# Kernel optimization log

Measured on AMD Instinct MI355X. Metric: run time of the kernel, lower is better.

## Reference

```python
import jax, jax.numpy as jnp
import numpy as np

B, CIN, COUT, H, W = 16, 128, 128, 64, 64
K1, K2, DIL = 3, 3, 1
PAD0 = DIL * (K1 - 1) // 2
PAD1 = DIL * (K2 - 1) // 2
L = H * W


def setup_inputs() -> dict:
    key = jax.random.key(0)
    k1, k2, k3, k4, k5 = jax.random.split(key, 5)
    x = jax.random.normal(k1, (B, CIN, H, W), dtype=jnp.float32)
    # binary per-pixel mask over kernel taps, broadcast over batch*channels
    mask = (jax.random.uniform(k2, (1, K1 * K2, L)) < 0.5).astype(jnp.float32)
    fan_in = CIN * K1 * K2
    bound = 1.0 / np.sqrt(fan_in)
    weight = jax.random.uniform(k3, (COUT, CIN, K1, K2), jnp.float32, -bound, bound)
    mask_weight = jax.random.uniform(k4, (COUT, K1, K2), jnp.float32, -bound, bound)
    bias = jax.random.uniform(k5, (COUT,), jnp.float32, -bound, bound)
    return {"x": x, "mask": mask, "weight": weight, "mask_weight": mask_weight, "bias": bias}


def reference(x, mask, weight, mask_weight, bias):
    # im2col: [B, CIN*K1*K2, H, W]; channel ordering (cin, k1, k2) matches torch unfold
    patches = jax.lax.conv_general_dilated_patches(
        x, (K1, K2), (1, 1), [(PAD0, PAD0), (PAD1, PAD1)], rhs_dilation=(DIL, DIL))
    p = patches.reshape(B, CIN, K1 * K2, L)
    p = p * mask[:, None, :, :]          # mask [1, K, L] broadcasts over B and CIN
    p = p.reshape(B, CIN * K1 * K2, L)
    out = jnp.einsum('ok,bkl->bol', weight.reshape(COUT, -1), p)
    out = out + bias[None, :, None]
    out = out + jnp.einsum('ok,mkl->mol', mask_weight.reshape(COUT, -1), mask)
    return out.reshape(B, COUT, H, W)
```

## Files before the change

kernel.cpp:

```cpp
#include <hip/hip_runtime.h>
#include <stdint.h>

#define B_    16
#define CIN_  128
#define COUT_ 128
#define H_    64
#define W_    64
#define L_    4096
#define KK_   1152
#define PW_   66
#define PPIX_ (PW_ * PW_)

typedef unsigned short u16;
typedef __bf16 bf16x8 __attribute__((ext_vector_type(8)));
typedef float  floatx4 __attribute__((ext_vector_type(4)));
typedef uint32_t u32x4 __attribute__((ext_vector_type(4)));

typedef const __attribute__((address_space(1))) uint32_t* gptr_t;
typedef __attribute__((address_space(3))) uint32_t*       lptr_t;

__device__ __forceinline__ void async_copy16(const void* g, void* l) {
    __builtin_amdgcn_global_load_lds((gptr_t)g, (lptr_t)l, 16, 0, 0);
}

__device__ __forceinline__ u16 f2bf(float f) {
    uint32_t u = __builtin_bit_cast(uint32_t, f);
    uint32_t r = u + 0x7FFFu + ((u >> 16) & 1u);
    return (u16)(r >> 16);
}

__global__ void lmc_prep_kernel(const float* __restrict__ x,
                                const float* __restrict__ mask, const float* __restrict__ mw,
                                const float* __restrict__ bias, const float* __restrict__ w,
                                u16* __restrict__ xTp, float* __restrict__ mb,
                                u16* __restrict__ wb2) {
    const int bid = blockIdx.x, tid = threadIdx.x;
    if (bid < 1024) {
        __shared__ u16 tile[64][CIN_ + 8];
        const int b = bid >> 6;
        const int y = bid & 63;

        {
            const int c  = tid >> 1;
            const int x0 = (tid & 1) * 32;
            const float* src = x + ((size_t)b * CIN_ + c) * L_ + y * 64 + x0;
            #pragma unroll
            for (int j = 0; j < 32; j += 4) {
                float4 v = *reinterpret_cast<const float4*>(src + j);
                tile[x0 + j + 0][c] = f2bf(v.x);
                tile[x0 + j + 1][c] = f2bf(v.y);
                tile[x0 + j + 2][c] = f2bf(v.z);
                tile[x0 + j + 3][c] = f2bf(v.w);
            }
        }
        __syncthreads();

        u16* dstrow = xTp + ((size_t)(b * PW_ + (y + 1)) * PW_) * CIN_;
        {
            const int xx   = tid >> 2;
            const int cseg = (tid & 3) * 32;
            u16* dst = dstrow + (size_t)(xx + 1) * CIN_ + cseg;
            #pragma unroll
            for (int i = 0; i < 32; i += 8) {
                *reinterpret_cast<uint4*>(dst + i) =
                    *reinterpret_cast<const uint4*>(&tile[xx][cseg + i]);
            }
        }
        const uint4 z = {0u, 0u, 0u, 0u};
        if (tid < 32) {
            const int pix = (tid >> 4) ? 65 : 0;
            *reinterpret_cast<uint4*>(dstrow + (size_t)pix * CIN_ + (tid & 15) * 8) = z;
        }
        if (y == 0 || y == 63) {
            u16* brow = xTp + ((size_t)(b * PW_ + (y == 0 ? 0 : 65)) * PW_) * CIN_;
            for (int i = tid; i < (PW_ * CIN_) / 8; i += 256)
                reinterpret_cast<uint4*>(brow)[i] = z;
        }
    } else if (bid < 1152) {
        const int o = bid - 1024;
        float m[9];
        #pragma unroll
        for (int k = 0; k < 9; ++k) m[k] = mw[o * 9 + k];
        const float bs = bias[o];
        for (int l = tid; l < L_; l += 256) {
            float s = bs;
            #pragma unroll
            for (int k = 0; k < 9; ++k) s += m[k] * mask[k * L_ + l];
            mb[o * L_ + l] = s;
        }
    } else {
        const int base = (bid - 1152) * 2304;
        #pragma unroll
        for (int i = 0; i < 9; ++i) {
            const int e = base + i * 256 + tid;
            const int k = e >> 14;
            const int rem = e & 16383;
            const int o = rem >> 7, c = rem & 127;
            wb2[e] = f2bf(w[(size_t)o * KK_ + c * 9 + k]);
        }
    }
}

__global__ __launch_bounds__(512, 2)
void lmc_gemm_kernel(const u16* __restrict__ xTp, const u16* __restrict__ wb2,
                     const float* __restrict__ mask, const float* __restrict__ mb,
                     float* __restrict__ out) {
    __shared__ u16 W_lds[396 * 128];
    __shared__ u16 A_lds[3][128 * 64];

    const int flat    = blockIdx.x;
    const int logical = (flat & 7) * 32 + (flat >> 3);
    const int b       = logical >> 4;
    const int lt      = logical & 15;
    const int Y       = lt * 4;
    const int l0      = lt * 256;

    const int tid  = threadIdx.x;
    const int lane = tid & 63;
    const int wv   = tid >> 6;
    const int wm   = (wv >> 2) * 64;
    const int wn   = (wv & 3) * 64;
    const int lrow = lane & 15;
    const int quad = lane >> 4;

    const char* wb2_c = (const char*)wb2;
    char* A_c = (char*)A_lds;

    {
        const char* xw = (const char*)xTp + ((size_t)(b * PW_ + Y) * PW_) * 256;
        for (int t = wv; t < 99; t += 8) {
            const int p    = t * 4 + quad;
            const int srcc = lrow ^ (p & 7);
            async_copy16(xw + (size_t)p * 256 + srcc * 16,
                         (char*)W_lds + t * 1024);
        }
    }

    const int ao  = (lane >> 3);
    const int ach = (lane & 7) ^ (ao & 7);
    const int aoff0 = (8 * wv + ao) * 256 + ach * 16;
    async_copy16(wb2_c + aoff0,              A_c + wv * 1024);
    async_copy16(wb2_c + aoff0 + 16384,      A_c + wv * 1024 + 8192);
    async_copy16(wb2_c + 128 + aoff0,        A_c + 16384 + wv * 1024);
    async_copy16(wb2_c + 128 + aoff0 + 16384, A_c + 16384 + wv * 1024 + 8192);

    int pix0[4];
    uint64_t bits = 0;
    #pragma unroll
    for (int j = 0; j < 4; ++j) {
        const int ll = wn + j * 16 + lrow;
        pix0[j] = ((ll >> 6) + 1) * 66 + (ll & 63) + 1;
        const int lg = l0 + ll;
        #pragma unroll
        for (int k = 0; k < 9; ++k)
            if (mask[k * L_ + lg] != 0.0f) bits |= (1ull << (k * 4 + j));
    }

    floatx4 acc[4][4];
    #pragma unroll
    for (int i = 0; i < 4; ++i)
        #pragma unroll
        for (int j = 0; j < 4; ++j)
            acc[i][j] = (floatx4){0.f, 0.f, 0.f, 0.f};

    asm volatile("s_waitcnt vmcnt(2)" ::: "memory");
    __builtin_amdgcn_s_barrier();
    asm volatile("" ::: "memory");

    int bufr = 0;
    int bufw = 2;
    for (int g = 0; g < 18; ++g) {
        const int k = g >> 1;

        if (g < 16) {
            const int gn   = g + 2;
            const int koff = (gn >> 1) * 32768 + (gn & 1) * 128;
            char* dstb = A_c + bufw * 16384;
            async_copy16(wb2_c + koff + aoff0,         dstb + wv * 1024);
            async_copy16(wb2_c + koff + aoff0 + 16384, dstb + wv * 1024 + 8192);
        }

        const int sh = (k / 3 - 1) * 66 + (k % 3) - 1;
        uint32_t kp[4];
        #pragma unroll
        for (int j = 0; j < 4; ++j)
            kp[j] = 0u - (uint32_t)((bits >> (k * 4 + j)) & 1ull);

        const u16* Ac = (const u16*)(A_c + bufr * 16384);

        #pragma unroll
        for (int ksl = 0; ksl < 2; ++ksl) {
            const int ksg = (g & 1) * 2 + ksl;
            bf16x8 af[4], bf[4];
            #pragma unroll
            for (int i = 0; i < 4; ++i) {
                const int orow = wm + i * 16 + lrow;
                const int slot = (ksl * 4 + quad) ^ (orow & 7);
                af[i] = *reinterpret_cast<const bf16x8*>(&Ac[orow * 64 + slot * 8]);
            }
            #pragma unroll
            for (int j = 0; j < 4; ++j) {
                const int pix  = pix0[j] + sh;
                const int slot = (ksg * 4 + quad) ^ (pix & 7);
                bf16x8 v = *reinterpret_cast<const bf16x8*>(&W_lds[pix * 128 + slot * 8]);
                u32x4 t = __builtin_bit_cast(u32x4, v);
                t &= kp[j];
                bf[j] = __builtin_bit_cast(bf16x8, t);
            }
            __builtin_amdgcn_s_setprio(1);
            #pragma unroll
            for (int i = 0; i < 4; ++i)
                #pragma unroll
                for (int j = 0; j < 4; ++j)
                    acc[i][j] = __builtin_amdgcn_mfma_f32_16x16x32_bf16(
                        af[i], bf[j], acc[i][j], 0, 0, 0);
            __builtin_amdgcn_s_setprio(0);
        }

        if (g < 16) {
            asm volatile("s_waitcnt vmcnt(2)" ::: "memory");
            __builtin_amdgcn_s_barrier();
            asm volatile("" ::: "memory");
        } else if (g == 16) {
            asm volatile("s_waitcnt vmcnt(0)" ::: "memory");
            __builtin_amdgcn_s_barrier();
            asm volatile("" ::: "memory");
        }
        bufr = (bufr == 2) ? 0 : bufr + 1;
        bufw = (bufw == 2) ? 0 : bufw + 1;
    }

    #pragma unroll
    for (int i = 0; i < 4; ++i) {
        #pragma unroll
        for (int j = 0; j < 4; ++j) {
            const int l = l0 + wn + j * 16 + lrow;
            #pragma unroll
            for (int r = 0; r < 4; ++r) {
                const int o = wm + i * 16 + quad * 4 + r;
                out[((size_t)b * COUT_ + o) * L_ + l] = acc[i][j][r] + mb[o * L_ + l];
            }
        }
    }
}

extern "C" void kernel_launch(void* const* d_in, const int* in_sizes, int n_in,
                              void* d_out, int out_size, void* d_ws, size_t ws_size,
                              hipStream_t stream) {
    const float* x      = (const float*)d_in[0];
    const float* mask   = (const float*)d_in[1];
    const float* weight = (const float*)d_in[2];
    const float* mw     = (const float*)d_in[3];
    const float* bias   = (const float*)d_in[4];
    float* out = (float*)d_out;

    char* ws = (char*)d_ws;
    u16*   xTp = (u16*)ws;
    u16*   wb2 = (u16*)(ws + 17842176);
    float* mb  = (float*)(ws + 17842176 + 294912);

    lmc_prep_kernel<<<1216, 256, 0, stream>>>(x, mask, mw, bias, weight, xTp, mb, wb2);
    lmc_gemm_kernel<<<256, 512, 0, stream>>>(xTp, wb2, mask, mb, out);
}
```

Baseline: 124.7 us.

## Fuse prep and GEMM kernels into one cooperative kernel with grid sync

Merges the separate prep kernel (bf16 transpose/padding of x, mask-bias precompute, weight reorder) into the GEMM kernel. Each of the 256 blocks does its share of the prep work and then waits at a grid-wide barrier before the GEMM phase. This is meant to remove one kernel launch and the gap between the two kernels. In exchange, prep now runs on only 256 blocks instead of 1216, and the grid barrier adds a synchronization cost.

```diff
diff --git a/kernel.cpp b/kernel.cpp
--- a/kernel.cpp
+++ b/kernel.cpp
@@ -1,5 +1,8 @@
 #include <hip/hip_runtime.h>
+#include <hip/hip_cooperative_groups.h>
 #include <stdint.h>
+
+namespace cg = cooperative_groups;
 
 #define B_    16
 #define CIN_  128
@@ -29,82 +32,12 @@
     return (u16)(r >> 16);
 }
 
-__global__ void lmc_prep_kernel(const float* __restrict__ x,
-                                const float* __restrict__ mask, const float* __restrict__ mw,
-                                const float* __restrict__ bias, const float* __restrict__ w,
-                                u16* __restrict__ xTp, float* __restrict__ mb,
-                                u16* __restrict__ wb2) {
-    const int bid = blockIdx.x, tid = threadIdx.x;
-    if (bid < 1024) {
-        __shared__ u16 tile[64][CIN_ + 8];
-        const int b = bid >> 6;
-        const int y = bid & 63;
-
-        {
-            const int c  = tid >> 1;
-            const int x0 = (tid & 1) * 32;
-            const float* src = x + ((size_t)b * CIN_ + c) * L_ + y * 64 + x0;
-            #pragma unroll
-            for (int j = 0; j < 32; j += 4) {
-                float4 v = *reinterpret_cast<const float4*>(src + j);
-                tile[x0 + j + 0][c] = f2bf(v.x);
-                tile[x0 + j + 1][c] = f2bf(v.y);
-                tile[x0 + j + 2][c] = f2bf(v.z);
-                tile[x0 + j + 3][c] = f2bf(v.w);
-            }
-        }
-        __syncthreads();
-
-        u16* dstrow = xTp + ((size_t)(b * PW_ + (y + 1)) * PW_) * CIN_;
-        {
-            const int xx   = tid >> 2;
-            const int cseg = (tid & 3) * 32;
-            u16* dst = dstrow + (size_t)(xx + 1) * CIN_ + cseg;
-            #pragma unroll
-            for (int i = 0; i < 32; i += 8) {
-                *reinterpret_cast<uint4*>(dst + i) =
-                    *reinterpret_cast<const uint4*>(&tile[xx][cseg + i]);
-            }
-        }
-        const uint4 z = {0u, 0u, 0u, 0u};
-        if (tid < 32) {
-            const int pix = (tid >> 4) ? 65 : 0;
-            *reinterpret_cast<uint4*>(dstrow + (size_t)pix * CIN_ + (tid & 15) * 8) = z;
-        }
-        if (y == 0 || y == 63) {
-            u16* brow = xTp + ((size_t)(b * PW_ + (y == 0 ? 0 : 65)) * PW_) * CIN_;
-            for (int i = tid; i < (PW_ * CIN_) / 8; i += 256)
-                reinterpret_cast<uint4*>(brow)[i] = z;
-        }
-    } else if (bid < 1152) {
-        const int o = bid - 1024;
-        float m[9];
-        #pragma unroll
-        for (int k = 0; k < 9; ++k) m[k] = mw[o * 9 + k];
-        const float bs = bias[o];
-        for (int l = tid; l < L_; l += 256) {
-            float s = bs;
-            #pragma unroll
-            for (int k = 0; k < 9; ++k) s += m[k] * mask[k * L_ + l];
-            mb[o * L_ + l] = s;
-        }
-    } else {
-        const int base = (bid - 1152) * 2304;
-        #pragma unroll
-        for (int i = 0; i < 9; ++i) {
-            const int e = base + i * 256 + tid;
-            const int k = e >> 14;
-            const int rem = e & 16383;
-            const int o = rem >> 7, c = rem & 127;
-            wb2[e] = f2bf(w[(size_t)o * KK_ + c * 9 + k]);
-        }
-    }
-}
-
 __global__ __launch_bounds__(512, 2)
-void lmc_gemm_kernel(const u16* __restrict__ xTp, const u16* __restrict__ wb2,
-                     const float* __restrict__ mask, const float* __restrict__ mb,
-                     float* __restrict__ out) {
+void lmc_fused_kernel(const float* __restrict__ x,
+                      const float* __restrict__ mask, const float* __restrict__ mw,
+                      const float* __restrict__ bias, const float* __restrict__ w,
+                      u16* __restrict__ xTp, float* __restrict__ mb,
+                      u16* __restrict__ wb2, float* __restrict__ out) {
     __shared__ u16 W_lds[396 * 128];
     __shared__ u16 A_lds[3][128 * 64];
 
@@ -123,6 +56,82 @@
     const int lrow = lane & 15;
     const int quad = lane >> 4;
 
+    {
+        u16* tile = (u16*)W_lds;
+        const uint4 z = {0u, 0u, 0u, 0u};
+        for (int r = 0; r < 4; ++r) {
+            const int y = Y + r;
+            {
+                const int c  = tid >> 2;
+                const int x0 = (tid & 3) * 16;
+                const float* src = x + ((size_t)b * CIN_ + c) * L_ + y * 64 + x0;
+                #pragma unroll
+                for (int j = 0; j < 16; j += 4) {
+                    float4 v = *reinterpret_cast<const float4*>(src + j);
+                    tile[(x0 + j + 0) * 136 + c] = f2bf(v.x);
+                    tile[(x0 + j + 1) * 136 + c] = f2bf(v.y);
+                    tile[(x0 + j + 2) * 136 + c] = f2bf(v.z);
+                    tile[(x0 + j + 3) * 136 + c] = f2bf(v.w);
+                }
+            }
+            __syncthreads();
+            u16* dstrow = xTp + ((size_t)(b * PW_ + (y + 1)) * PW_) * CIN_;
+            {
+                const int xx = tid >> 3;
+                const int cs = (tid & 7) * 16;
+                u16* dst = dstrow + (size_t)(xx + 1) * CIN_ + cs;
+                *reinterpret_cast<uint4*>(dst)     = *reinterpret_cast<const uint4*>(&tile[xx * 136 + cs]);
+                *reinterpret_cast<uint4*>(dst + 8) = *reinterpret_cast<const uint4*>(&tile[xx * 136 + cs + 8]);
+            }
+            if (tid < 32) {
+                const int pix = (tid >> 4) ? 65 : 0;
+                *reinterpret_cast<uint4*>(dstrow + (size_t)pix * CIN_ + (tid & 15) * 8) = z;
+            }
+            __syncthreads();
+        }
+        if (lt == 0 || lt == 15) {
+            u16* brow = xTp + ((size_t)(b * PW_ + (lt == 0 ? 0 : 65)) * PW_) * CIN_;
+            for (int i = tid; i < (PW_ * CIN_) / 8; i += 512)
+                reinterpret_cast<uint4*>(brow)[i] = z;
+        }
+    }
+
+    {
+        const int o  = flat >> 1;
+        const int l  = (flat & 1) * 2048 + tid * 4;
+        float m[9];
+        #pragma unroll
+        for (int k = 0; k < 9; ++k) m[k] = mw[o * 9 + k];
+        const float bs = bias[o];
+        float4 s = {bs, bs, bs, bs};
+        #pragma unroll
+        for (int k = 0; k < 9; ++k) {
+            float4 mk = *reinterpret_cast<const float4*>(&mask[k * L_ + l]);
+            s.x += m[k] * mk.x;  s.y += m[k] * mk.y;
+            s.z += m[k] * mk.z;  s.w += m[k] * mk.w;
+        }
+        *reinterpret_cast<float4*>(&mb[o * L_ + l]) = s;
+    }
+
+    {
+        const int e0 = flat * 576 + tid;
+        {
+            const int e = e0;
+            const int k = e >> 14, rem = e & 16383;
+            const int o = rem >> 7, c = rem & 127;
+            wb2[e] = f2bf(w[(size_t)o * KK_ + c * 9 + k]);
+        }
+        if (tid < 64) {
+            const int e = e0 + 512;
+            const int k = e >> 14, rem = e & 16383;
+            const int o = rem >> 7, c = rem & 127;
+            wb2[e] = f2bf(w[(size_t)o * KK_ + c * 9 + k]);
+        }
+    }
+
+    __threadfence();
+    cg::this_grid().sync();
+
     const char* wb2_c = (const char*)wb2;
     char* A_c = (char*)A_lds;
 
@@ -139,9 +148,9 @@
     const int ao  = (lane >> 3);
     const int ach = (lane & 7) ^ (ao & 7);
     const int aoff0 = (8 * wv + ao) * 256 + ach * 16;
-    async_copy16(wb2_c + aoff0,              A_c + wv * 1024);
-    async_copy16(wb2_c + aoff0 + 16384,      A_c + wv * 1024 + 8192);
-    async_copy16(wb2_c + 128 + aoff0,        A_c + 16384 + wv * 1024);
+    async_copy16(wb2_c + aoff0,               A_c + wv * 1024);
+    async_copy16(wb2_c + aoff0 + 16384,       A_c + wv * 1024 + 8192);
+    async_copy16(wb2_c + 128 + aoff0,         A_c + 16384 + wv * 1024);
     async_copy16(wb2_c + 128 + aoff0 + 16384, A_c + 16384 + wv * 1024 + 8192);
 
     int pix0[4];
@@ -259,6 +268,8 @@
     u16*   wb2 = (u16*)(ws + 17842176);
     float* mb  = (float*)(ws + 17842176 + 294912);
 
-    lmc_prep_kernel<<<1216, 256, 0, stream>>>(x, mask, mw, bias, weight, xTp, mb, wb2);
-    lmc_gemm_kernel<<<256, 512, 0, stream>>>(xTp, wb2, mask, mb, out);
-}
+    void* args[] = {(void*)&x, (void*)&mask, (void*)&mw, (void*)&bias, (void*)&weight,
+                    (void*)&xTp, (void*)&mb, (void*)&wb2, (void*)&out};
+    hipLaunchCooperativeKernel((const void*)lmc_fused_kernel,
+                               dim3(256), dim3(512), args, 0, stream);
+}
```

Measured after the change: 225.9 us. +81.2%, slower.

## Fuse x bf16 transpose/padding into GEMM kernel, loading fp32 x directly into LDS

Applied to the files above, without the earlier changes.

Removes the prep-kernel stage that converted x to a padded, channel-last bf16 buffer in workspace. The GEMM kernel now reads fp32 x directly, converts it to bf16 in registers and writes it swizzled into LDS, zeroing the halo itself. This drops a full write and re-read of the intermediate tensor and shrinks the prep launch. In exchange the input load is synchronous instead of async-to-LDS, so it no longer overlaps with the first weight loads. Halo rows are also read redundantly across tiles.

```diff
diff --git a/kernel.cpp b/kernel.cpp
--- a/kernel.cpp
+++ b/kernel.cpp
@@ -8,8 +8,6 @@
 #define W_    64
 #define L_    4096
 #define KK_   1152
-#define PW_   66
-#define PPIX_ (PW_ * PW_)
 
 typedef unsigned short u16;
 typedef __bf16 bf16x8 __attribute__((ext_vector_type(8)));
@@ -29,55 +27,12 @@
     return (u16)(r >> 16);
 }
 
-__global__ void lmc_prep_kernel(const float* __restrict__ x,
-                                const float* __restrict__ mask, const float* __restrict__ mw,
+__global__ void lmc_prep_kernel(const float* __restrict__ mask, const float* __restrict__ mw,
                                 const float* __restrict__ bias, const float* __restrict__ w,
-                                u16* __restrict__ xTp, float* __restrict__ mb,
-                                u16* __restrict__ wb2) {
+                                float* __restrict__ mb, u16* __restrict__ wb2) {
     const int bid = blockIdx.x, tid = threadIdx.x;
-    if (bid < 1024) {
-        __shared__ u16 tile[64][CIN_ + 8];
-        const int b = bid >> 6;
-        const int y = bid & 63;
-
-        {
-            const int c  = tid >> 1;
-            const int x0 = (tid & 1) * 32;
-            const float* src = x + ((size_t)b * CIN_ + c) * L_ + y * 64 + x0;
-            #pragma unroll
-            for (int j = 0; j < 32; j += 4) {
-                float4 v = *reinterpret_cast<const float4*>(src + j);
-                tile[x0 + j + 0][c] = f2bf(v.x);
-                tile[x0 + j + 1][c] = f2bf(v.y);
-                tile[x0 + j + 2][c] = f2bf(v.z);
-                tile[x0 + j + 3][c] = f2bf(v.w);
-            }
-        }
-        __syncthreads();
-
-        u16* dstrow = xTp + ((size_t)(b * PW_ + (y + 1)) * PW_) * CIN_;
-        {
-            const int xx   = tid >> 2;
-            const int cseg = (tid & 3) * 32;
-            u16* dst = dstrow + (size_t)(xx + 1) * CIN_ + cseg;
-            #pragma unroll
-            for (int i = 0; i < 32; i += 8) {
-                *reinterpret_cast<uint4*>(dst + i) =
-                    *reinterpret_cast<const uint4*>(&tile[xx][cseg + i]);
-            }
-        }
-        const uint4 z = {0u, 0u, 0u, 0u};
-        if (tid < 32) {
-            const int pix = (tid >> 4) ? 65 : 0;
-            *reinterpret_cast<uint4*>(dstrow + (size_t)pix * CIN_ + (tid & 15) * 8) = z;
-        }
-        if (y == 0 || y == 63) {
-            u16* brow = xTp + ((size_t)(b * PW_ + (y == 0 ? 0 : 65)) * PW_) * CIN_;
-            for (int i = tid; i < (PW_ * CIN_) / 8; i += 256)
-                reinterpret_cast<uint4*>(brow)[i] = z;
-        }
-    } else if (bid < 1152) {
-        const int o = bid - 1024;
+    if (bid < 128) {
+        const int o = bid;
         float m[9];
         #pragma unroll
         for (int k = 0; k < 9; ++k) m[k] = mw[o * 9 + k];
@@ -89,7 +44,7 @@
             mb[o * L_ + l] = s;
         }
     } else {
-        const int base = (bid - 1152) * 2304;
+        const int base = (bid - 128) * 2304;
         #pragma unroll
         for (int i = 0; i < 9; ++i) {
             const int e = base + i * 256 + tid;
@@ -102,7 +57,7 @@
 }
 
 __global__ __launch_bounds__(512, 2)
-void lmc_gemm_kernel(const u16* __restrict__ xTp, const u16* __restrict__ wb2,
+void lmc_gemm_kernel(const float* __restrict__ x, const u16* __restrict__ wb2,
                      const float* __restrict__ mask, const float* __restrict__ mb,
                      float* __restrict__ out) {
     __shared__ u16 W_lds[396 * 128];
@@ -123,26 +78,55 @@
     const int lrow = lane & 15;
     const int quad = lane >> 4;
 
-    const char* wb2_c = (const char*)wb2;
-    char* A_c = (char*)A_lds;
-
+    if (tid < 192) {
+        const int h  = tid >> 4;
+        const int px = (h >> 1) * 66 + ((h & 1) ? 65 : 0);
+        const uint4 z = {0u, 0u, 0u, 0u};
+        *reinterpret_cast<uint4*>((char*)W_lds + px * 256 + (tid & 15) * 16) = z;
+    }
     {
-        const char* xw = (const char*)xTp + ((size_t)(b * PW_ + Y) * PW_) * 256;
-        for (int t = wv; t < 99; t += 8) {
-            const int p    = t * 4 + quad;
-            const int srcc = lrow ^ (p & 7);
-            async_copy16(xw + (size_t)p * 256 + srcc * 16,
-                         (char*)W_lds + t * 1024);
-        }
-    }
-
-    const int ao  = (lane >> 3);
-    const int ach = (lane & 7) ^ (ao & 7);
-    const int aoff0 = (8 * wv + ao) * 256 + ach * 16;
-    async_copy16(wb2_c + aoff0,              A_c + wv * 1024);
-    async_copy16(wb2_c + aoff0 + 16384,      A_c + wv * 1024 + 8192);
-    async_copy16(wb2_c + 128 + aoff0,        A_c + 16384 + wv * 1024);
-    async_copy16(wb2_c + 128 + aoff0 + 16384, A_c + 16384 + wv * 1024 + 8192);
+        const int cg  = lane >> 4;
+        const int x0  = (lane & 15) * 4;
+        const int cb  = wv;
+        const int cbase = cb * 16 + cg * 4;
+        const int d     = cb * 2 + (cg >> 1);
+        const int half8 = (cg & 1) * 8;
+        const float* xc = x + ((size_t)(b * CIN_ + cbase) * L_) + x0;
+
+        #pragma unroll
+        for (int wy = 0; wy < 6; ++wy) {
+            const int y   = Y - 1 + wy;
+            const int px0 = wy * 66 + x0 + 1;
+            if (y >= 0 && y <= 63) {
+                const float* xr = xc + y * 64;
+                float4 v0 = *reinterpret_cast<const float4*>(xr);
+                float4 v1 = *reinterpret_cast<const float4*>(xr + L_);
+                float4 v2 = *reinterpret_cast<const float4*>(xr + 2 * L_);
+                float4 v3 = *reinterpret_cast<const float4*>(xr + 3 * L_);
+                const float* p0 = (const float*)&v0;
+                const float* p1 = (const float*)&v1;
+                const float* p2 = (const float*)&v2;
+                const float* p3 = (const float*)&v3;
+                #pragma unroll
+                for (int j = 0; j < 4; ++j) {
+                    const int px   = px0 + j;
+                    const int slot = d ^ (px & 7);
+                    uint2 pk;
+                    pk.x = (uint32_t)f2bf(p0[j]) | ((uint32_t)f2bf(p1[j]) << 16);
+                    pk.y = (uint32_t)f2bf(p2[j]) | ((uint32_t)f2bf(p3[j]) << 16);
+                    *reinterpret_cast<uint2*>((char*)W_lds + px * 256 + slot * 16 + half8) = pk;
+                }
+            } else {
+                const uint2 z2 = {0u, 0u};
+                #pragma unroll
+                for (int j = 0; j < 4; ++j) {
+                    const int px   = px0 + j;
+                    const int slot = d ^ (px & 7);
+                    *reinterpret_cast<uint2*>((char*)W_lds + px * 256 + slot * 16 + half8) = z2;
+                }
+            }
+        }
+    }
 
     int pix0[4];
     uint64_t bits = 0;
@@ -156,6 +140,16 @@
             if (mask[k * L_ + lg] != 0.0f) bits |= (1ull << (k * 4 + j));
     }
 
+    const char* wb2_c = (const char*)wb2;
+    char* A_c = (char*)A_lds;
+    const int ao  = (lane >> 3);
+    const int ach = (lane & 7) ^ (ao & 7);
+    const int aoff0 = (8 * wv + ao) * 256 + ach * 16;
+    async_copy16(wb2_c + aoff0,               A_c + wv * 1024);
+    async_copy16(wb2_c + aoff0 + 16384,       A_c + wv * 1024 + 8192);
+    async_copy16(wb2_c + 128 + aoff0,         A_c + 16384 + wv * 1024);
+    async_copy16(wb2_c + 128 + aoff0 + 16384, A_c + 16384 + wv * 1024 + 8192);
+
     floatx4 acc[4][4];
     #pragma unroll
     for (int i = 0; i < 4; ++i)
@@ -163,7 +157,7 @@
         for (int j = 0; j < 4; ++j)
             acc[i][j] = (floatx4){0.f, 0.f, 0.f, 0.f};
 
-    asm volatile("s_waitcnt vmcnt(2)" ::: "memory");
+    asm volatile("s_waitcnt vmcnt(2) lgkmcnt(0)" ::: "memory");
     __builtin_amdgcn_s_barrier();
     asm volatile("" ::: "memory");
 
@@ -255,10 +249,9 @@
     float* out = (float*)d_out;
 
     char* ws = (char*)d_ws;
-    u16*   xTp = (u16*)ws;
-    u16*   wb2 = (u16*)(ws + 17842176);
-    float* mb  = (float*)(ws + 17842176 + 294912);
-
-    lmc_prep_kernel<<<1216, 256, 0, stream>>>(x, mask, mw, bias, weight, xTp, mb, wb2);
-    lmc_gemm_kernel<<<256, 512, 0, stream>>>(xTp, wb2, mask, mb, out);
-}
+    u16*   wb2 = (u16*)ws;
+    float* mb  = (float*)(ws + 294912);
+
+    lmc_prep_kernel<<<192, 256, 0, stream>>>(mask, mw, bias, weight, mb, wb2);
+    lmc_gemm_kernel<<<256, 512, 0, stream>>>(x, wb2, mask, mb, out);
+}
```

After: 118.5 us. 1.05x faster.
